# Kernel tuning notes

Measured on AMD Instinct MI355X. Metric: run time of the kernel, lower is better.

The kernel has to match this reference:

```python
import jax, jax.numpy as jnp
import numpy as np

B, L, D, H = 4, 2048, 1024, 16
HD = D // H
NEG = -1e9  # stands in for -inf in masks; identical softmax result, grad-safe
EPS = 1e-5


def _layer_norm(x, g, b):
    mu = jnp.mean(x, axis=-1, keepdims=True)
    var = jnp.mean((x - mu) ** 2, axis=-1, keepdims=True)
    return (x - mu) * jax.lax.rsqrt(var + EPS) * g + b


def setup_inputs() -> dict:
    key = jax.random.key(0)
    ks = jax.random.split(key, 8)
    x = jax.random.normal(ks[0], (B, L, D), dtype=jnp.float32)
    # length-based padding: valid lengths in [L//2, L]; True = padded position
    lengths = jax.random.randint(ks[1], (B,), L // 2, L + 1)
    padding_mask = jnp.arange(L)[None, :] >= lengths[:, None]  # (B, L) bool
    # additive causal mask: 0 on/below diagonal, NEG above
    causal_mask = jnp.where(jnp.tril(jnp.ones((L, L), dtype=bool)), 0.0, NEG).astype(jnp.float32)

    def linear_params(k, fan_in, fan_out):
        bound = float(np.sqrt(6.0 / (fan_in + fan_out)))  # xavier_uniform
        W = jax.random.uniform(k, (fan_out, fan_in), jnp.float32, -bound, bound)
        b = jnp.zeros((fan_out,), jnp.float32)
        return W, b

    Wq, bq = linear_params(ks[2], D, D)
    Wk, bk = linear_params(ks[3], D, D)
    Wv, bv = linear_params(ks[4], D, D)
    Wo, bo = linear_params(ks[5], D, D)
    g_pre = jnp.ones((D,), jnp.float32); b_pre = jnp.zeros((D,), jnp.float32)
    g_ln = jnp.ones((D,), jnp.float32); b_ln = jnp.zeros((D,), jnp.float32)
    return {
        "x": x, "padding_mask": padding_mask, "causal_mask": causal_mask,
        "Wq": Wq, "bq": bq, "Wk": Wk, "bk": bk, "Wv": Wv, "bv": bv,
        "Wo": Wo, "bo": bo, "g_pre": g_pre, "b_pre": b_pre,
        "g_ln": g_ln, "b_ln": b_ln,
    }


def reference(x, padding_mask, causal_mask, Wq, bq, Wk, bk, Wv, bv, Wo, bo,
              g_pre, b_pre, g_ln, b_ln):
    # pre-LayerNorm (residual uses the normed x, matching the torch code)
    h = _layer_norm(x, g_pre, b_pre)  # (B, L, D)

    def heads(W, b):
        y = jnp.einsum('bld,ed->ble', h, W) + b           # torch Linear: x @ W.T + b
        return y.reshape(B, L, H, HD).transpose(0, 2, 1, 3)  # (B, H, L, HD)

    q, k, v = heads(Wq, bq), heads(Wk, bk), heads(Wv, bv)

    scores = jnp.einsum('bhld,bhmd->bhlm', q, k) / jnp.sqrt(jnp.float32(HD))
    scores = scores + causal_mask  # additive causal mask broadcast over (B, H)
    # padding mask: True = masked key position
    scores = jnp.where(padding_mask[:, None, None, :], NEG, scores)
    attn = jax.nn.softmax(scores, axis=-1)  # dropout p=0.0 (eval / disabled)

    out = jnp.einsum('bhlm,bhmd->bhld', attn, v)          # (B, H, L, HD)
    out = out.transpose(0, 2, 1, 3).reshape(B, L, D)
    out = jnp.einsum('bld,ed->ble', out, Wo) + bo
    return _layer_norm(out + h, g_ln, b_ln)
```

## Files before the change

kernel.cpp:

```cpp
#include <hip/hip_runtime.h>


#define Bq 4
#define Lq 2048
#define Dq 1024
#define Hq 16
#define HDq 64
#define Mq (Bq * Lq)

typedef __attribute__((ext_vector_type(8))) short short8;
typedef __attribute__((ext_vector_type(4))) float f32x4;
typedef __attribute__((address_space(3))) unsigned char lds_byte;
typedef __attribute__((address_space(1))) unsigned char gbl_byte;

__device__ __forceinline__ unsigned short f2b(float f) {
    unsigned int u = __float_as_uint(f);
    unsigned int r = (u + 0x7fffu + ((u >> 16) & 1u)) >> 16;
    return (unsigned short)r;
}
__device__ __forceinline__ float b2f(unsigned short u) {
    return __uint_as_float(((unsigned int)u) << 16);
}
__device__ __forceinline__ unsigned int packbf(float lo, float hi) {
    return (unsigned int)f2b(lo) | ((unsigned int)f2b(hi) << 16);
}

#define GLL16(gsrc, ldst)                                              \
    __builtin_amdgcn_global_load_lds((const gbl_byte*)(gsrc),          \
                                     (lds_byte*)(ldst), 16, 0, 0)

__global__ void setup_kernel(const unsigned char* __restrict__ m8,
                             int* __restrict__ lengths) {
    __shared__ int bad;
    __shared__ int fo[4];
    const int tid = threadIdx.x;
    if (tid == 0) bad = 0;
    if (tid < 4) fo[tid] = Lq;
    __syncthreads();
    for (int i = tid; i < Bq * Lq; i += 256) {
        unsigned char v = m8[i];
        if (v) {
            int r = i >> 11, c = i & (Lq - 1);
            atomicMin(&fo[r], c);
            if (c < Lq / 2) atomicOr(&bad, 1);
            else if (c < Lq - 1 && m8[i + 1] == 0) atomicOr(&bad, 1);
        }
    }
    __syncthreads();
    int anyone = (fo[0] < Lq) | (fo[1] < Lq) | (fo[2] < Lq) | (fo[3] < Lq);
    bool use8 = (bad == 0) && anyone;
    if (!use8) {
        __syncthreads();
        if (tid < 4) fo[tid] = Lq;
        __syncthreads();
        const int* m32 = (const int*)m8;
        for (int i = tid; i < Bq * Lq; i += 256) {
            if (m32[i] != 0) atomicMin(&fo[i >> 11], i & (Lq - 1));
        }
        __syncthreads();
    }
    if (tid < 4) lengths[tid] = fo[tid];
}

__global__ __launch_bounds__(256) void cvt4_kernel(
    const float* __restrict__ s0, const float* __restrict__ s1,
    const float* __restrict__ s2, const float* __restrict__ s3,
    unsigned short* __restrict__ dst) {
    const int region = blockIdx.x >> 10;
    const int i = (blockIdx.x & 1023) * 256 + threadIdx.x;
    const float* src = (region == 0) ? s0 : (region == 1) ? s1
                       : (region == 2) ? s2 : s3;
    float4 v = ((const float4*)src)[i];
    ushort4 o;
    o.x = f2b(v.x); o.y = f2b(v.y); o.z = f2b(v.z); o.w = f2b(v.w);
    ((ushort4*)dst)[(size_t)region * (Dq * Dq / 4) + i] = o;
}

__global__ __launch_bounds__(256) void ln_pre_kernel(
    const float* __restrict__ x, const float* __restrict__ g,
    const float* __restrict__ bb, unsigned short* __restrict__ out) {
    const int row = blockIdx.x, tid = threadIdx.x;
    float4 u = ((const float4*)x)[(size_t)row * 256 + tid];
    float s = u.x + u.y + u.z + u.w;
    float ss = u.x * u.x + u.y * u.y + u.z * u.z + u.w * u.w;
#pragma unroll
    for (int off = 32; off > 0; off >>= 1) {
        s += __shfl_xor(s, off);
        ss += __shfl_xor(ss, off);
    }
    __shared__ float sred[4], ssred[4];
    const int w = tid >> 6, lane = tid & 63;
    if (lane == 0) { sred[w] = s; ssred[w] = ss; }
    __syncthreads();
    s = sred[0] + sred[1] + sred[2] + sred[3];
    ss = ssred[0] + ssred[1] + ssred[2] + ssred[3];
    const float mean = s * (1.f / Dq);
    const float rstd = rsqrtf(ss * (1.f / Dq) - mean * mean + 1e-5f);
    float4 gv = ((const float4*)g)[tid];
    float4 bv = ((const float4*)bb)[tid];
    ushort4 o;
    o.x = f2b((u.x - mean) * rstd * gv.x + bv.x);
    o.y = f2b((u.y - mean) * rstd * gv.y + bv.y);
    o.z = f2b((u.z - mean) * rstd * gv.z + bv.z);
    o.w = f2b((u.w - mean) * rstd * gv.w + bv.w);
    ((ushort4*)out)[(size_t)row * 256 + tid] = o;
}

__global__ __launch_bounds__(256) void qkv_gemm_kernel(
    const unsigned short* __restrict__ A, const unsigned short* __restrict__ W3,
    const float* __restrict__ bq, const float* __restrict__ bk,
    const float* __restrict__ bv, unsigned short* __restrict__ Qo,
    unsigned short* __restrict__ Ko, unsigned short* __restrict__ Vto) {
    __shared__ unsigned short As[128][32];
    __shared__ unsigned short Bs[128][32];
    const int tid = threadIdx.x;
    const int w = tid >> 6, lane = tid & 63;
    const int lm = lane & 15, lq = lane >> 4;
    const int m0 = blockIdx.y << 7, n0 = blockIdx.x << 7;
    const int wm = (w >> 1) << 6, wn = (w & 1) << 6;
    f32x4 acc[4][4];
#pragma unroll
    for (int i = 0; i < 4; ++i)
#pragma unroll
        for (int j = 0; j < 4; ++j) acc[i][j] = (f32x4){0.f, 0.f, 0.f, 0.f};
    for (int k0 = 0; k0 < Dq; k0 += 32) {
        __syncthreads();
#pragma unroll
        for (int j = 0; j < 2; ++j) {
            const int base = j * 256 + w * 64;
            const int slot = base + lane;
            const int row = slot >> 2, c = slot & 3;
            GLL16(A + (size_t)(m0 + row) * Dq + k0 + c * 8,
                  (unsigned short*)As + base * 8);
            GLL16(W3 + (size_t)(n0 + row) * Dq + k0 + c * 8,
                  (unsigned short*)Bs + base * 8);
        }
        __syncthreads();
        short8 af[4], bf[4];
#pragma unroll
        for (int t = 0; t < 4; ++t)
            af[t] = *(const short8*)&As[wm + t * 16 + lm][lq * 8];
#pragma unroll
        for (int t = 0; t < 4; ++t)
            bf[t] = *(const short8*)&Bs[wn + t * 16 + lm][lq * 8];
#pragma unroll
        for (int mt = 0; mt < 4; ++mt)
#pragma unroll
            for (int nt = 0; nt < 4; ++nt)
                acc[mt][nt] = __builtin_amdgcn_mfma_f32_16x16x32_bf16(
                    af[mt], bf[nt], acc[mt][nt], 0, 0, 0);
    }
    const int region = n0 >> 10;
    const float* bias = (region == 0) ? bq : (region == 1) ? bk : bv;
    const float scale = (region == 0) ? 0.125f : 1.0f;
    const int nb = n0 & 1023;
#pragma unroll
    for (int nt = 0; nt < 4; ++nt) {
        const int colb = nb + wn + nt * 16 + lm;
        const float bval = bias[colb];
#pragma unroll
        for (int mt = 0; mt < 4; ++mt) {
            const int row0 = m0 + wm + mt * 16 + lq * 4;
            const int bidx = row0 >> 11, l0r = row0 & (Lq - 1);
            if (region < 2) {
                unsigned short* dst = (region == 0) ? Qo : Ko;
#pragma unroll
                for (int r = 0; r < 4; ++r)
                    dst[((size_t)(bidx * Hq + (colb >> 6)) * Lq + l0r + r) *
                            HDq + (colb & 63)] =
                        f2b((acc[mt][nt][r] + bval) * scale);
            } else {
                ushort4 o;
                o.x = f2b(acc[mt][nt][0] + bval);
                o.y = f2b(acc[mt][nt][1] + bval);
                o.z = f2b(acc[mt][nt][2] + bval);
                o.w = f2b(acc[mt][nt][3] + bval);
                *(ushort4*)&Vto[((size_t)(bidx * Hq + (colb >> 6)) * HDq +
                                 (colb & 63)) * Lq + l0r] = o;
            }
        }
    }
}

__global__ __launch_bounds__(256) void proj_gemm_kernel(
    const unsigned short* __restrict__ A, const unsigned short* __restrict__ Bw,
    const float* __restrict__ bias, float* __restrict__ Cout) {
    __shared__ unsigned short As[128][32];
    __shared__ unsigned short Bs[128][32];
    const int tid = threadIdx.x;
    const int w = tid >> 6, lane = tid & 63;
    const int lm = lane & 15, lq = lane >> 4;
    const int m0 = blockIdx.y << 7, n0 = blockIdx.x << 7;
    const int wm = (w >> 1) << 6, wn = (w & 1) << 6;
    f32x4 acc[4][4];
#pragma unroll
    for (int i = 0; i < 4; ++i)
#pragma unroll
        for (int j = 0; j < 4; ++j) acc[i][j] = (f32x4){0.f, 0.f, 0.f, 0.f};
    for (int k0 = 0; k0 < Dq; k0 += 32) {
        __syncthreads();
#pragma unroll
        for (int j = 0; j < 2; ++j) {
            const int base = j * 256 + w * 64;
            const int slot = base + lane;
            const int row = slot >> 2, c = slot & 3;
            const int rr = m0 + row, kk = k0 + c * 8;
            GLL16(A + ((size_t)((rr >> 11) * Hq + (kk >> 6)) * Lq +
                       (rr & (Lq - 1))) * HDq + (kk & 63),
                  (unsigned short*)As + base * 8);
            GLL16(Bw + (size_t)(n0 + row) * Dq + k0 + c * 8,
                  (unsigned short*)Bs + base * 8);
        }
        __syncthreads();
        short8 af[4], bf[4];
#pragma unroll
        for (int t = 0; t < 4; ++t)
            af[t] = *(const short8*)&As[wm + t * 16 + lm][lq * 8];
#pragma unroll
        for (int t = 0; t < 4; ++t)
            bf[t] = *(const short8*)&Bs[wn + t * 16 + lm][lq * 8];
#pragma unroll
        for (int mt = 0; mt < 4; ++mt)
#pragma unroll
            for (int nt = 0; nt < 4; ++nt)
                acc[mt][nt] = __builtin_amdgcn_mfma_f32_16x16x32_bf16(
                    af[mt], bf[nt], acc[mt][nt], 0, 0, 0);
    }
#pragma unroll
    for (int nt = 0; nt < 4; ++nt) {
        const float bval = bias[n0 + wn + nt * 16 + lm];
#pragma unroll
        for (int mt = 0; mt < 4; ++mt)
#pragma unroll
            for (int r = 0; r < 4; ++r)
                Cout[(size_t)(m0 + wm + mt * 16 + lq * 4 + r) * Dq + n0 + wn +
                     nt * 16 + lm] = acc[mt][nt][r] + bval;
    }
}

__global__ __launch_bounds__(256) void attn_kernel(
    const unsigned short* __restrict__ Qg, const unsigned short* __restrict__ Kg,
    const unsigned short* __restrict__ Vtg, const int* __restrict__ lengths,
    unsigned short* __restrict__ Og) {
    __shared__ unsigned short Ps[4][16][72];
    const int bx = blockIdx.x;
    const int hh = blockIdx.y, b = blockIdx.z;
    const int tid = threadIdx.x, w = tid >> 6, lane = tid & 63;
    const int lm = lane & 15, lq = lane >> 4;
    const int len = lengths[b];
    const int mxk = (len + 63) >> 6;
    const size_t hb = (size_t)(b * Hq + hh) * Lq * HDq;
    const unsigned short* Vb = Vtg + hb;

#pragma unroll
    for (int pass = 0; pass < 2; ++pass) {
        const int qt = pass ? bx : (15 - bx);
        const int l0 = qt << 7;
        short8 qf[2][2];
#pragma unroll
        for (int s = 0; s < 2; ++s)
#pragma unroll
            for (int h = 0; h < 2; ++h)
                qf[s][h] = *(const short8*)(Qg + hb +
                    (size_t)(l0 + w * 32 + s * 16 + lm) * HDq + h * 32 + lq * 8);
        f32x4 oacc[2][4];
        float m_i[2], l_i[2];
#pragma unroll
        for (int s = 0; s < 2; ++s) {
            m_i[s] = -1e30f; l_i[s] = 0.f;
#pragma unroll
            for (int t = 0; t < 4; ++t)
                oacc[s][t] = (f32x4){0.f, 0.f, 0.f, 0.f};
        }
        int nkt = 2 * qt + 2;
        if (nkt > mxk) nkt = mxk;
        for (int kt = 0; kt < nkt; ++kt) {
            const int kb = kt << 6;
            short8 kf[4][2], vf[4][2];
#pragma unroll
            for (int t = 0; t < 4; ++t)
#pragma unroll
                for (int h = 0; h < 2; ++h)
                    kf[t][h] = *(const short8*)(Kg + hb +
                        (size_t)(kb + t * 16 + lm) * HDq + h * 32 + lq * 8);
#pragma unroll
            for (int t = 0; t < 4; ++t)
#pragma unroll
                for (int kh = 0; kh < 2; ++kh)
                    vf[t][kh] = *(const short8*)(Vb +
                        (size_t)(t * 16 + lm) * Lq + kb + kh * 32 + lq * 8);
#pragma unroll
            for (int s = 0; s < 2; ++s) {
                f32x4 sc[4];
#pragma unroll
                for (int t = 0; t < 4; ++t) {
                    f32x4 z = (f32x4){0.f, 0.f, 0.f, 0.f};
                    z = __builtin_amdgcn_mfma_f32_16x16x32_bf16(
                        kf[t][0], qf[s][0], z, 0, 0, 0);
                    z = __builtin_amdgcn_mfma_f32_16x16x32_bf16(
                        kf[t][1], qf[s][1], z, 0, 0, 0);
                    sc[t] = z;
                }
                const int qmin = l0 + w * 32 + s * 16;
                float pvv[16];
                float mx = -1e30f;
                if ((kb + 63 <= qmin) && (kb + 63 < len)) {
#pragma unroll
                    for (int i = 0; i < 16; ++i) {
                        const float v = sc[i >> 2][i & 3];
                        pvv[i] = v;
                        mx = fmaxf(mx, v);
                    }
                } else {
                    const int q = qmin + lm;
#pragma unroll
                    for (int t = 0; t < 4; ++t)
#pragma unroll
                        for (int r = 0; r < 4; ++r) {
                            const int key = kb + t * 16 + lq * 4 + r;
                            float v = sc[t][r];
                            if (key > q || key >= len) v = -1e30f;
                            pvv[t * 4 + r] = v;
                            mx = fmaxf(mx, v);
                        }
                }
                mx = fmaxf(mx, __shfl_xor(mx, 16));
                mx = fmaxf(mx, __shfl_xor(mx, 32));
                const float mnew = fmaxf(m_i[s], mx);
                const float alpha = __expf(m_i[s] - mnew);
                m_i[s] = mnew;
                float psum = 0.f;
#pragma unroll
                for (int i = 0; i < 16; ++i) {
                    const float p = __expf(pvv[i] - mnew);
                    pvv[i] = p;
                    psum += p;
                }
                psum += __shfl_xor(psum, 16);
                psum += __shfl_xor(psum, 32);
                l_i[s] = l_i[s] * alpha + psum;
#pragma unroll
                for (int t = 0; t < 4; ++t) {
                    oacc[s][t][0] *= alpha; oacc[s][t][1] *= alpha;
                    oacc[s][t][2] *= alpha; oacc[s][t][3] *= alpha;
                }
#pragma unroll
                for (int t = 0; t < 4; ++t) {
                    uint2 uu;
                    uu.x = packbf(pvv[t * 4 + 0], pvv[t * 4 + 1]);
                    uu.y = packbf(pvv[t * 4 + 2], pvv[t * 4 + 3]);
                    *(uint2*)&Ps[w][lm][t * 16 + lq * 4] = uu;
                }
                asm volatile("s_waitcnt lgkmcnt(0)" ::: "memory");
                short8 pf0 = *(const short8*)&Ps[w][lm][lq * 8];
                short8 pf1 = *(const short8*)&Ps[w][lm][32 + lq * 8];
#pragma unroll
                for (int t = 0; t < 4; ++t) {
                    oacc[s][t] = __builtin_amdgcn_mfma_f32_16x16x32_bf16(
                        vf[t][0], pf0, oacc[s][t], 0, 0, 0);
                    oacc[s][t] = __builtin_amdgcn_mfma_f32_16x16x32_bf16(
                        vf[t][1], pf1, oacc[s][t], 0, 0, 0);
                }
            }
        }
#pragma unroll
        for (int s = 0; s < 2; ++s) {
            const float inv = 1.f / l_i[s];
            unsigned short* Ot =
                Og + hb + (size_t)(l0 + w * 32 + s * 16 + lm) * HDq;
#pragma unroll
            for (int t = 0; t < 4; ++t) {
                ushort4 o;
                o.x = f2b(oacc[s][t][0] * inv);
                o.y = f2b(oacc[s][t][1] * inv);
                o.z = f2b(oacc[s][t][2] * inv);
                o.w = f2b(oacc[s][t][3] * inv);
                *(ushort4*)(Ot + t * 16 + lq * 4) = o;
            }
        }
    }
}

__global__ __launch_bounds__(256) void ln_final_kernel(
    const float* __restrict__ pj, const unsigned short* __restrict__ h,
    const float* __restrict__ g, const float* __restrict__ bb,
    float* __restrict__ out) {
    const int row = blockIdx.x, tid = threadIdx.x;
    float4 a = ((const float4*)pj)[(size_t)row * 256 + tid];
    ushort4 hv = ((const ushort4*)h)[(size_t)row * 256 + tid];
    float f0 = a.x + b2f(hv.x), f1 = a.y + b2f(hv.y);
    float f2 = a.z + b2f(hv.z), f3 = a.w + b2f(hv.w);
    float s = f0 + f1 + f2 + f3;
    float ss = f0 * f0 + f1 * f1 + f2 * f2 + f3 * f3;
#pragma unroll
    for (int off = 32; off > 0; off >>= 1) {
        s += __shfl_xor(s, off);
        ss += __shfl_xor(ss, off);
    }
    __shared__ float sred[4], ssred[4];
    const int w = tid >> 6, lane = tid & 63;
    if (lane == 0) { sred[w] = s; ssred[w] = ss; }
    __syncthreads();
    s = sred[0] + sred[1] + sred[2] + sred[3];
    ss = ssred[0] + ssred[1] + ssred[2] + ssred[3];
    const float mean = s * (1.f / Dq);
    const float rstd = rsqrtf(ss * (1.f / Dq) - mean * mean + 1e-5f);
    float4 gv = ((const float4*)g)[tid];
    float4 bv = ((const float4*)bb)[tid];
    float4 o;
    o.x = (f0 - mean) * rstd * gv.x + bv.x;
    o.y = (f1 - mean) * rstd * gv.y + bv.y;
    o.z = (f2 - mean) * rstd * gv.z + bv.z;
    o.w = (f3 - mean) * rstd * gv.w + bv.w;
    ((float4*)out)[(size_t)row * 256 + tid] = o;
}

extern "C" void kernel_launch(void* const* d_in, const int* in_sizes, int n_in,
                              void* d_out, int out_size, void* d_ws,
                              size_t ws_size, hipStream_t stream) {
    const float* x = (const float*)d_in[0];
    const unsigned char* mask = (const unsigned char*)d_in[1];
    const float* Wq = (const float*)d_in[3];
    const float* bq = (const float*)d_in[4];
    const float* Wk = (const float*)d_in[5];
    const float* bk = (const float*)d_in[6];
    const float* Wv = (const float*)d_in[7];
    const float* bvv = (const float*)d_in[8];
    const float* Wo = (const float*)d_in[9];
    const float* bo = (const float*)d_in[10];
    const float* g_pre = (const float*)d_in[11];
    const float* b_pre = (const float*)d_in[12];
    const float* g_ln = (const float*)d_in[13];
    const float* b_ln = (const float*)d_in[14];

    const size_t SZ = (size_t)Mq * Dq;
    const size_t WSZ = (size_t)Dq * Dq;
    unsigned short* h = (unsigned short*)d_ws;
    unsigned short* q = h + SZ;
    unsigned short* k = q + SZ;
    unsigned short* vT = k + SZ;
    unsigned short* at = vT + SZ;
    unsigned short* W3 = at + SZ;
    unsigned short* wob = W3 + 3 * WSZ;
    float* proj = (float*)(wob + WSZ);
    int* lengths = (int*)(proj + SZ);

    setup_kernel<<<1, 256, 0, stream>>>(mask, lengths);
    cvt4_kernel<<<4096, 256, 0, stream>>>(Wq, Wk, Wv, Wo, W3);
    ln_pre_kernel<<<Mq, 256, 0, stream>>>(x, g_pre, b_pre, h);

    qkv_gemm_kernel<<<dim3(3 * Dq / 128, Mq / 128), 256, 0, stream>>>(
        h, W3, bq, bk, bvv, q, k, vT);
    attn_kernel<<<dim3(Lq / 256, Hq, Bq), 256, 0, stream>>>(q, k, vT, lengths,
                                                            at);
    proj_gemm_kernel<<<dim3(Dq / 128, Mq / 128), 256, 0, stream>>>(at, wob, bo,
                                                                   proj);
    ln_final_kernel<<<Mq, 256, 0, stream>>>(proj, h, g_ln, b_ln,
                                            (float*)d_out);
}
```

Measured before the change: 408.6 us.

## Halve attention block work to 16 rows per wave and skip redundant rescale

The attention grid doubles from 8 to 16 blocks along the sequence, and each wave now handles 16 query rows instead of 32. Each block pairs two 64-row halves of complementary query tiles to balance causal work. Rows past the diagonal also drop one key tile, since nkt now follows the 64-row half. The online-softmax rescale of the accumulator is skipped when no lane's max increased. This buys more parallelism and occupancy at the cost of reloading K/V tiles once per 16 rows instead of per 32, doubling K/V traffic per query row.

```diff
diff --git a/kernel.cpp b/kernel.cpp
--- a/kernel.cpp
+++ b/kernel.cpp
@@ -244,6 +244,7 @@
     unsigned short* __restrict__ Og) {
     __shared__ unsigned short Ps[4][16][72];
     const int bx = blockIdx.x;
+    const int pp = bx & 7, b2 = bx >> 3;
     const int hh = blockIdx.y, b = blockIdx.z;
     const int tid = threadIdx.x, w = tid >> 6, lane = tid & 63;
     const int lm = lane & 15, lq = lane >> 4;
@@ -254,25 +255,19 @@
 
 #pragma unroll
     for (int pass = 0; pass < 2; ++pass) {
-        const int qt = pass ? bx : (15 - bx);
-        const int l0 = qt << 7;
-        short8 qf[2][2];
-#pragma unroll
-        for (int s = 0; s < 2; ++s)
-#pragma unroll
-            for (int h = 0; h < 2; ++h)
-                qf[s][h] = *(const short8*)(Qg + hb +
-                    (size_t)(l0 + w * 32 + s * 16 + lm) * HDq + h * 32 + lq * 8);
-        f32x4 oacc[2][4];
-        float m_i[2], l_i[2];
-#pragma unroll
-        for (int s = 0; s < 2; ++s) {
-            m_i[s] = -1e30f; l_i[s] = 0.f;
-#pragma unroll
-            for (int t = 0; t < 4; ++t)
-                oacc[s][t] = (f32x4){0.f, 0.f, 0.f, 0.f};
-        }
-        int nkt = 2 * qt + 2;
+        const int qt = pass ? pp : (15 - pp);
+        const int h2 = pass ? (1 - b2) : b2;
+        const int r0 = (qt << 7) + (h2 << 6) + w * 16;
+        short8 qf[2];
+#pragma unroll
+        for (int h = 0; h < 2; ++h)
+            qf[h] = *(const short8*)(Qg + hb + (size_t)(r0 + lm) * HDq +
+                                     h * 32 + lq * 8);
+        f32x4 oacc[4];
+        float m_i = -1e30f, l_i = 0.f;
+#pragma unroll
+        for (int t = 0; t < 4; ++t) oacc[t] = (f32x4){0.f, 0.f, 0.f, 0.f};
+        int nkt = 2 * qt + h2 + 1;
         if (nkt > mxk) nkt = mxk;
         for (int kt = 0; kt < nkt; ++kt) {
             const int kb = kt << 6;
@@ -289,94 +284,89 @@
                 for (int kh = 0; kh < 2; ++kh)
                     vf[t][kh] = *(const short8*)(Vb +
                         (size_t)(t * 16 + lm) * Lq + kb + kh * 32 + lq * 8);
-#pragma unroll
-            for (int s = 0; s < 2; ++s) {
-                f32x4 sc[4];
-#pragma unroll
-                for (int t = 0; t < 4; ++t) {
-                    f32x4 z = (f32x4){0.f, 0.f, 0.f, 0.f};
-                    z = __builtin_amdgcn_mfma_f32_16x16x32_bf16(
-                        kf[t][0], qf[s][0], z, 0, 0, 0);
-                    z = __builtin_amdgcn_mfma_f32_16x16x32_bf16(
-                        kf[t][1], qf[s][1], z, 0, 0, 0);
-                    sc[t] = z;
+            f32x4 sc[4];
+#pragma unroll
+            for (int t = 0; t < 4; ++t) {
+                f32x4 z = (f32x4){0.f, 0.f, 0.f, 0.f};
+                z = __builtin_amdgcn_mfma_f32_16x16x32_bf16(
+                    kf[t][0], qf[0], z, 0, 0, 0);
+                z = __builtin_amdgcn_mfma_f32_16x16x32_bf16(
+                    kf[t][1], qf[1], z, 0, 0, 0);
+                sc[t] = z;
+            }
+            float pvv[16];
+            float mx = -1e30f;
+            if ((kb + 63 <= r0) && (kb + 63 < len)) {
+#pragma unroll
+                for (int i = 0; i < 16; ++i) {
+                    const float v = sc[i >> 2][i & 3];
+                    pvv[i] = v;
+                    mx = fmaxf(mx, v);
                 }
-                const int qmin = l0 + w * 32 + s * 16;
-                float pvv[16];
-                float mx = -1e30f;
-                if ((kb + 63 <= qmin) && (kb + 63 < len)) {
-#pragma unroll
-                    for (int i = 0; i < 16; ++i) {
-                        const float v = sc[i >> 2][i & 3];
-                        pvv[i] = v;
+            } else {
+                const int q = r0 + lm;
+#pragma unroll
+                for (int t = 0; t < 4; ++t)
+#pragma unroll
+                    for (int r = 0; r < 4; ++r) {
+                        const int key = kb + t * 16 + lq * 4 + r;
+                        float v = sc[t][r];
+                        if (key > q || key >= len) v = -1e30f;
+                        pvv[t * 4 + r] = v;
                         mx = fmaxf(mx, v);
                     }
-                } else {
-                    const int q = qmin + lm;
-#pragma unroll
-                    for (int t = 0; t < 4; ++t)
-#pragma unroll
-                        for (int r = 0; r < 4; ++r) {
-                            const int key = kb + t * 16 + lq * 4 + r;
-                            float v = sc[t][r];
-                            if (key > q || key >= len) v = -1e30f;
-                            pvv[t * 4 + r] = v;
-                            mx = fmaxf(mx, v);
-                        }
+            }
+            mx = fmaxf(mx, __shfl_xor(mx, 16));
+            mx = fmaxf(mx, __shfl_xor(mx, 32));
+            const float mnew = fmaxf(m_i, mx);
+            float psum = 0.f;
+#pragma unroll
+            for (int i = 0; i < 16; ++i) {
+                const float p = __expf(pvv[i] - mnew);
+                pvv[i] = p;
+                psum += p;
+            }
+#pragma unroll
+            for (int t = 0; t < 4; ++t) {
+                uint2 uu;
+                uu.x = packbf(pvv[t * 4 + 0], pvv[t * 4 + 1]);
+                uu.y = packbf(pvv[t * 4 + 2], pvv[t * 4 + 3]);
+                *(uint2*)&Ps[w][lm][t * 16 + lq * 4] = uu;
+            }
+            psum += __shfl_xor(psum, 16);
+            psum += __shfl_xor(psum, 32);
+            if (__any(mx > m_i)) {
+                const float alpha = __expf(m_i - mnew);
+                m_i = mnew;
+                l_i *= alpha;
+#pragma unroll
+                for (int t = 0; t < 4; ++t) {
+                    oacc[t][0] *= alpha; oacc[t][1] *= alpha;
+                    oacc[t][2] *= alpha; oacc[t][3] *= alpha;
                 }
-                mx = fmaxf(mx, __shfl_xor(mx, 16));
-                mx = fmaxf(mx, __shfl_xor(mx, 32));
-                const float mnew = fmaxf(m_i[s], mx);
-                const float alpha = __expf(m_i[s] - mnew);
-                m_i[s] = mnew;
-                float psum = 0.f;
-#pragma unroll
-                for (int i = 0; i < 16; ++i) {
-                    const float p = __expf(pvv[i] - mnew);
-                    pvv[i] = p;
-                    psum += p;
-                }
-                psum += __shfl_xor(psum, 16);
-                psum += __shfl_xor(psum, 32);
-                l_i[s] = l_i[s] * alpha + psum;
-#pragma unroll
-                for (int t = 0; t < 4; ++t) {
-                    oacc[s][t][0] *= alpha; oacc[s][t][1] *= alpha;
-                    oacc[s][t][2] *= alpha; oacc[s][t][3] *= alpha;
-                }
-#pragma unroll
-                for (int t = 0; t < 4; ++t) {
-                    uint2 uu;
-                    uu.x = packbf(pvv[t * 4 + 0], pvv[t * 4 + 1]);
-                    uu.y = packbf(pvv[t * 4 + 2], pvv[t * 4 + 3]);
-                    *(uint2*)&Ps[w][lm][t * 16 + lq * 4] = uu;
-                }
-                asm volatile("s_waitcnt lgkmcnt(0)" ::: "memory");
-                short8 pf0 = *(const short8*)&Ps[w][lm][lq * 8];
-                short8 pf1 = *(const short8*)&Ps[w][lm][32 + lq * 8];
-#pragma unroll
-                for (int t = 0; t < 4; ++t) {
-                    oacc[s][t] = __builtin_amdgcn_mfma_f32_16x16x32_bf16(
-                        vf[t][0], pf0, oacc[s][t], 0, 0, 0);
-                    oacc[s][t] = __builtin_amdgcn_mfma_f32_16x16x32_bf16(
-                        vf[t][1], pf1, oacc[s][t], 0, 0, 0);
-                }
-            }
-        }
-#pragma unroll
-        for (int s = 0; s < 2; ++s) {
-            const float inv = 1.f / l_i[s];
-            unsigned short* Ot =
-                Og + hb + (size_t)(l0 + w * 32 + s * 16 + lm) * HDq;
+            }
+            l_i += psum;
+            asm volatile("s_waitcnt lgkmcnt(0)" ::: "memory");
+            short8 pf0 = *(const short8*)&Ps[w][lm][lq * 8];
+            short8 pf1 = *(const short8*)&Ps[w][lm][32 + lq * 8];
 #pragma unroll
             for (int t = 0; t < 4; ++t) {
-                ushort4 o;
-                o.x = f2b(oacc[s][t][0] * inv);
-                o.y = f2b(oacc[s][t][1] * inv);
-                o.z = f2b(oacc[s][t][2] * inv);
-                o.w = f2b(oacc[s][t][3] * inv);
-                *(ushort4*)(Ot + t * 16 + lq * 4) = o;
-            }
+                oacc[t] = __builtin_amdgcn_mfma_f32_16x16x32_bf16(
+                    vf[t][0], pf0, oacc[t], 0, 0, 0);
+                oacc[t] = __builtin_amdgcn_mfma_f32_16x16x32_bf16(
+                    vf[t][1], pf1, oacc[t], 0, 0, 0);
+            }
+        }
+        const float inv = 1.f / l_i;
+        unsigned short* Ot = Og + hb + (size_t)(r0 + lm) * HDq;
+#pragma unroll
+        for (int t = 0; t < 4; ++t) {
+            ushort4 o;
+            o.x = f2b(oacc[t][0] * inv);
+            o.y = f2b(oacc[t][1] * inv);
+            o.z = f2b(oacc[t][2] * inv);
+            o.w = f2b(oacc[t][3] * inv);
+            *(ushort4*)(Ot + t * 16 + lq * 4) = o;
         }
     }
 }
@@ -451,7 +441,7 @@
 
     qkv_gemm_kernel<<<dim3(3 * Dq / 128, Mq / 128), 256, 0, stream>>>(
         h, W3, bq, bk, bvv, q, k, vT);
-    attn_kernel<<<dim3(Lq / 256, Hq, Bq), 256, 0, stream>>>(q, k, vT, lengths,
+    attn_kernel<<<dim3(Lq / 128, Hq, Bq), 256, 0, stream>>>(q, k, vT, lengths,
                                                             at);
     proj_gemm_kernel<<<dim3(Dq / 128, Mq / 128), 256, 0, stream>>>(at, wob, bo,
                                                                    proj);
```

After: 539.2 us. +32.0%, slower.

## Double-buffer K fragments in attention loop and add MFMA priority hints

Applied to the files above, without the earlier changes.

Restructures the attention key-tile loop into a two-way unrolled ping-pong so the K fragments for the next tile are loaded from global memory while the current tile's QK and PV MFMAs run. It also wraps the MFMA groups in s_setprio raises, reorders the softmax so the P stores to LDS are issued before the alpha rescale, and sets launch_bounds to two blocks per CU. This hides global load latency at the cost of more registers for the second K buffer, which the occupancy hint may force into spills.

```diff
diff --git a/kernel.cpp b/kernel.cpp
--- a/kernel.cpp
+++ b/kernel.cpp
@@ -28,6 +28,9 @@
 #define GLL16(gsrc, ldst)                                              \
     __builtin_amdgcn_global_load_lds((const gbl_byte*)(gsrc),          \
                                      (lds_byte*)(ldst), 16, 0, 0)
+
+#define MFMA_BF16(A, B, C) \
+    __builtin_amdgcn_mfma_f32_16x16x32_bf16((A), (B), (C), 0, 0, 0)
 
 __global__ void setup_kernel(const unsigned char* __restrict__ m8,
                              int* __restrict__ lengths) {
@@ -238,7 +241,108 @@
     }
 }
 
-__global__ __launch_bounds__(256) void attn_kernel(
+
+#define ATTN_KT_BODY(KT, KF, KFN)                                           \
+    {                                                                       \
+        const int kb = (KT) << 6;                                           \
+        short8 vf[4][2];                                                    \
+        _Pragma("unroll")                                                   \
+        for (int t = 0; t < 4; ++t) {                                       \
+            _Pragma("unroll")                                               \
+            for (int kh = 0; kh < 2; ++kh)                                  \
+                vf[t][kh] = *(const short8*)(Vb +                           \
+                    (size_t)(t * 16 + lm) * Lq + kb + kh * 32 + lq * 8);    \
+        }                                                                   \
+        if ((KT) + 1 < nkt) {                                               \
+            const int kb2 = kb + 64;                                        \
+            _Pragma("unroll")                                               \
+            for (int t = 0; t < 4; ++t) {                                   \
+                _Pragma("unroll")                                           \
+                for (int h = 0; h < 2; ++h)                                 \
+                    KFN[t][h] = *(const short8*)(Kg + hb +                  \
+                        (size_t)(kb2 + t * 16 + lm) * HDq + h * 32 +        \
+                        lq * 8);                                            \
+            }                                                               \
+        }                                                                   \
+        _Pragma("unroll")                                                   \
+        for (int s = 0; s < 2; ++s) {                                       \
+            f32x4 sc[4];                                                    \
+            __builtin_amdgcn_s_setprio(1);                                  \
+            _Pragma("unroll")                                               \
+            for (int t = 0; t < 4; ++t) {                                   \
+                f32x4 z = (f32x4){0.f, 0.f, 0.f, 0.f};                      \
+                z = MFMA_BF16(KF[t][0], qf[s][0], z);                       \
+                z = MFMA_BF16(KF[t][1], qf[s][1], z);                       \
+                sc[t] = z;                                                  \
+            }                                                               \
+            __builtin_amdgcn_s_setprio(0);                                  \
+            const int qmin = l0 + w * 32 + s * 16;                          \
+            float pvv[16];                                                  \
+            float mx = -1e30f;                                              \
+            if ((kb + 63 <= qmin) && (kb + 63 < len)) {                     \
+                _Pragma("unroll")                                           \
+                for (int i = 0; i < 16; ++i) {                              \
+                    const float v = sc[i >> 2][i & 3];                      \
+                    pvv[i] = v;                                             \
+                    mx = fmaxf(mx, v);                                      \
+                }                                                           \
+            } else {                                                        \
+                const int qq = qmin + lm;                                   \
+                _Pragma("unroll")                                           \
+                for (int t = 0; t < 4; ++t) {                               \
+                    _Pragma("unroll")                                       \
+                    for (int r = 0; r < 4; ++r) {                           \
+                        const int key = kb + t * 16 + lq * 4 + r;           \
+                        float v = sc[t][r];                                 \
+                        if (key > qq || key >= len) v = -1e30f;             \
+                        pvv[t * 4 + r] = v;                                 \
+                        mx = fmaxf(mx, v);                                  \
+                    }                                                       \
+                }                                                           \
+            }                                                               \
+            mx = fmaxf(mx, __shfl_xor(mx, 16));                            \
+            mx = fmaxf(mx, __shfl_xor(mx, 32));                            \
+            const float mnew = fmaxf(m_i[s], mx);                          \
+            float psum = 0.f;                                               \
+            _Pragma("unroll")                                               \
+            for (int i = 0; i < 16; ++i) {                                  \
+                const float p = __expf(pvv[i] - mnew);                      \
+                pvv[i] = p;                                                 \
+                psum += p;                                                  \
+            }                                                               \
+            _Pragma("unroll")                                               \
+            for (int t = 0; t < 4; ++t) {                                   \
+                uint2 uu;                                                   \
+                uu.x = packbf(pvv[t * 4 + 0], pvv[t * 4 + 1]);              \
+                uu.y = packbf(pvv[t * 4 + 2], pvv[t * 4 + 3]);              \
+                *(uint2*)&Ps[w][lm][t * 16 + lq * 4] = uu;                  \
+            }                                                               \
+            psum += __shfl_xor(psum, 16);                                   \
+            psum += __shfl_xor(psum, 32);                                   \
+            const float alpha = __expf(m_i[s] - mnew);                      \
+            m_i[s] = mnew;                                                  \
+            l_i[s] = l_i[s] * alpha + psum;                                 \
+            _Pragma("unroll")                                               \
+            for (int t = 0; t < 4; ++t) {                                   \
+                oacc[s][t][0] *= alpha;                                     \
+                oacc[s][t][1] *= alpha;                                     \
+                oacc[s][t][2] *= alpha;                                     \
+                oacc[s][t][3] *= alpha;                                     \
+            }                                                               \
+            asm volatile("s_waitcnt lgkmcnt(0)" ::: "memory");              \
+            short8 pf0 = *(const short8*)&Ps[w][lm][lq * 8];                \
+            short8 pf1 = *(const short8*)&Ps[w][lm][32 + lq * 8];           \
+            __builtin_amdgcn_s_setprio(1);                                  \
+            _Pragma("unroll")                                               \
+            for (int t = 0; t < 4; ++t) {                                   \
+                oacc[s][t] = MFMA_BF16(vf[t][0], pf0, oacc[s][t]);          \
+                oacc[s][t] = MFMA_BF16(vf[t][1], pf1, oacc[s][t]);          \
+            }                                                               \
+            __builtin_amdgcn_s_setprio(0);                                  \
+        }                                                                   \
+    }
+
+__global__ __launch_bounds__(256, 2) void attn_kernel(
     const unsigned short* __restrict__ Qg, const unsigned short* __restrict__ Kg,
     const unsigned short* __restrict__ Vtg, const int* __restrict__ lengths,
     unsigned short* __restrict__ Og) {
@@ -274,94 +378,21 @@
         }
         int nkt = 2 * qt + 2;
         if (nkt > mxk) nkt = mxk;
-        for (int kt = 0; kt < nkt; ++kt) {
-            const int kb = kt << 6;
-            short8 kf[4][2], vf[4][2];
-#pragma unroll
-            for (int t = 0; t < 4; ++t)
-#pragma unroll
-                for (int h = 0; h < 2; ++h)
-                    kf[t][h] = *(const short8*)(Kg + hb +
-                        (size_t)(kb + t * 16 + lm) * HDq + h * 32 + lq * 8);
-#pragma unroll
-            for (int t = 0; t < 4; ++t)
-#pragma unroll
-                for (int kh = 0; kh < 2; ++kh)
-                    vf[t][kh] = *(const short8*)(Vb +
-                        (size_t)(t * 16 + lm) * Lq + kb + kh * 32 + lq * 8);
-#pragma unroll
-            for (int s = 0; s < 2; ++s) {
-                f32x4 sc[4];
-#pragma unroll
-                for (int t = 0; t < 4; ++t) {
-                    f32x4 z = (f32x4){0.f, 0.f, 0.f, 0.f};
-                    z = __builtin_amdgcn_mfma_f32_16x16x32_bf16(
-                        kf[t][0], qf[s][0], z, 0, 0, 0);
-                    z = __builtin_amdgcn_mfma_f32_16x16x32_bf16(
-                        kf[t][1], qf[s][1], z, 0, 0, 0);
-                    sc[t] = z;
-                }
-                const int qmin = l0 + w * 32 + s * 16;
-                float pvv[16];
-                float mx = -1e30f;
-                if ((kb + 63 <= qmin) && (kb + 63 < len)) {
-#pragma unroll
-                    for (int i = 0; i < 16; ++i) {
-                        const float v = sc[i >> 2][i & 3];
-                        pvv[i] = v;
-                        mx = fmaxf(mx, v);
-                    }
-                } else {
-                    const int q = qmin + lm;
-#pragma unroll
-                    for (int t = 0; t < 4; ++t)
-#pragma unroll
-                        for (int r = 0; r < 4; ++r) {
-                            const int key = kb + t * 16 + lq * 4 + r;
-                            float v = sc[t][r];
-                            if (key > q || key >= len) v = -1e30f;
-                            pvv[t * 4 + r] = v;
-                            mx = fmaxf(mx, v);
-                        }
-                }
-                mx = fmaxf(mx, __shfl_xor(mx, 16));
-                mx = fmaxf(mx, __shfl_xor(mx, 32));
-                const float mnew = fmaxf(m_i[s], mx);
-                const float alpha = __expf(m_i[s] - mnew);
-                m_i[s] = mnew;
-                float psum = 0.f;
-#pragma unroll
-                for (int i = 0; i < 16; ++i) {
-                    const float p = __expf(pvv[i] - mnew);
-                    pvv[i] = p;
-                    psum += p;
-                }
-                psum += __shfl_xor(psum, 16);
-                psum += __shfl_xor(psum, 32);
-                l_i[s] = l_i[s] * alpha + psum;
-#pragma unroll
-                for (int t = 0; t < 4; ++t) {
-                    oacc[s][t][0] *= alpha; oacc[s][t][1] *= alpha;
-                    oacc[s][t][2] *= alpha; oacc[s][t][3] *= alpha;
-                }
-#pragma unroll
-                for (int t = 0; t < 4; ++t) {
-                    uint2 uu;
-                    uu.x = packbf(pvv[t * 4 + 0], pvv[t * 4 + 1]);
-                    uu.y = packbf(pvv[t * 4 + 2], pvv[t * 4 + 3]);
-                    *(uint2*)&Ps[w][lm][t * 16 + lq * 4] = uu;
-                }
-                asm volatile("s_waitcnt lgkmcnt(0)" ::: "memory");
-                short8 pf0 = *(const short8*)&Ps[w][lm][lq * 8];
-                short8 pf1 = *(const short8*)&Ps[w][lm][32 + lq * 8];
-#pragma unroll
-                for (int t = 0; t < 4; ++t) {
-                    oacc[s][t] = __builtin_amdgcn_mfma_f32_16x16x32_bf16(
-                        vf[t][0], pf0, oacc[s][t], 0, 0, 0);
-                    oacc[s][t] = __builtin_amdgcn_mfma_f32_16x16x32_bf16(
-                        vf[t][1], pf1, oacc[s][t], 0, 0, 0);
-                }
-            }
+        short8 kfa[4][2], kfb[4][2];
+#pragma unroll
+        for (int t = 0; t < 4; ++t)
+#pragma unroll
+            for (int h = 0; h < 2; ++h)
+                kfa[t][h] = *(const short8*)(Kg + hb +
+                    (size_t)(t * 16 + lm) * HDq + h * 32 + lq * 8);
+        int kt = 0;
+        for (;;) {
+            ATTN_KT_BODY(kt, kfa, kfb);
+            ++kt;
+            if (kt >= nkt) break;
+            ATTN_KT_BODY(kt, kfb, kfa);
+            ++kt;
+            if (kt >= nkt) break;
         }
 #pragma unroll
         for (int s = 0; s < 2; ++s) {
```

New measurement: 405.7 us. No clear change (-0.7%).
